# Kernel optimization log

Measured on AMD Instinct MI355X. Metric: run time of the kernel, lower is better.

The kernel has to match this reference:

```python
import jax, jax.numpy as jnp
import numpy as np

N_NODES = 100000
N_EDGES = 3200000
EMBED = 64
DIMS = [(64, 32), (32, 16)]  # (in_dim, out_dim) per Aggregator layer
EPS = 1e-12


def setup_inputs() -> dict:
    key = jax.random.key(0)
    ks = jax.random.split(key, 16)
    inp = {
        "aux_info_all": jax.random.normal(ks[0], (N_NODES, 3), jnp.float32),
        "entity_embed": jax.random.normal(ks[1], (N_NODES, EMBED), jnp.float32) * 0.1,
        "aux_W": jax.random.normal(ks[2], (EMBED, 3), jnp.float32) * 0.3,
        "aux_b": jnp.zeros((EMBED,), jnp.float32),
        "edge_vals": jax.random.uniform(ks[3], (N_EDGES,), jnp.float32),
        "edge_rows": jax.random.randint(ks[4], (N_EDGES,), 0, N_NODES, jnp.int32),
        "edge_cols": jax.random.randint(ks[5], (N_EDGES,), 0, N_NODES, jnp.int32),
    }
    for li, (din, dout) in enumerate(DIMS):
        s = (2.0 / (din + dout)) ** 0.5  # xavier-ish scale
        inp[f"W1_{li}"] = jax.random.normal(ks[6 + 4 * li], (dout, din), jnp.float32) * s
        inp[f"b1_{li}"] = jnp.zeros((dout,), jnp.float32)
        inp[f"W2_{li}"] = jax.random.normal(ks[7 + 4 * li], (dout, din), jnp.float32) * s
        inp[f"b2_{li}"] = jnp.zeros((dout,), jnp.float32)
    return inp


def _l2norm(x):
    return x / jnp.maximum(jnp.linalg.norm(x, axis=1, keepdims=True), EPS)


def reference(aux_info_all, entity_embed, aux_W, aux_b,
              W1_0, b1_0, W2_0, b2_0, W1_1, b1_1, W2_1, b2_1,
              edge_vals, edge_rows, edge_cols):
    # holographic fusion: entity_embed * (1 + tanh(Linear(aux)))
    aux_vec = jnp.tanh(aux_info_all @ aux_W.T + aux_b)
    ego = entity_embed * (1.0 + aux_vec)  # [N, 64]
    all_embed = [ego]
    layers = [(W1_0, b1_0, W2_0, b2_0), (W1_1, b1_1, W2_1, b2_1)]
    for W1, b1, W2, b2 in layers:
        # sparse A_in @ ego: gather messages over edges, segment-sum by destination row
        msgs = edge_vals[:, None] * ego[edge_cols]  # [E, d]
        side = jax.ops.segment_sum(msgs, edge_rows, num_segments=N_NODES)  # [N, d]
        sum_e = jax.nn.leaky_relu((ego + side) @ W1.T + b1)  # bi-interaction branch 1
        bi_e = jax.nn.leaky_relu((ego * side) @ W2.T + b2)   # bi-interaction branch 2
        ego = sum_e + bi_e  # (dropout p=0 in eval)
        all_embed.append(_l2norm(ego))
    return jnp.concatenate(all_embed, axis=1)  # [N, 64+32+16]
```

## Files before the change

### kernel.cpp

```cpp
#include <hip/hip_runtime.h>
#include <math.h>

#define NN 100000
#define NE 3200000
#define OUTD 112
#define BROWS 512
#define NBUCK 196
#define FILL_CH 8192
#define FILL_B ((NE + FILL_CH - 1) / FILL_CH)
#define BLD1_T 1024
#define SORT_T 512

__device__ inline unsigned short f32_to_bf16(float f) {
    unsigned u = __float_as_uint(f);
    u += 0x7FFFu + ((u >> 16) & 1u);
    return (unsigned short)(u >> 16);
}
__device__ inline float bf16_bits_to_f32(unsigned b) {
    return __uint_as_float(b << 16);
}

__global__ void fuse_ego_kernel(const float* __restrict__ aux_info,
                                const float* __restrict__ entity,
                                const float* __restrict__ aux_W,
                                const float* __restrict__ aux_b,
                                unsigned short* __restrict__ ego0h,
                                float* __restrict__ out) {
    int idx = blockIdx.x * blockDim.x + threadIdx.x;
    if (idx >= NN * 64) return;
    int n = idx >> 6;
    int j = idx & 63;
    float a0 = aux_info[n * 3 + 0];
    float a1 = aux_info[n * 3 + 1];
    float a2 = aux_info[n * 3 + 2];
    float w0 = aux_W[j * 3 + 0];
    float w1 = aux_W[j * 3 + 1];
    float w2 = aux_W[j * 3 + 2];
    float t = tanhf(fmaf(a0, w0, fmaf(a1, w1, fmaf(a2, w2, aux_b[j]))));
    float e = entity[idx] * (1.0f + t);
    ego0h[idx] = f32_to_bf16(e);
    out[(size_t)n * OUTD + j] = e;
}

__global__ void bhist_kernel(const int* __restrict__ rows, int* __restrict__ gcount) {
    __shared__ int h[NBUCK];
    for (int i = threadIdx.x; i < NBUCK; i += BLD1_T) h[i] = 0;
    __syncthreads();
    int base = blockIdx.x * FILL_CH;
    int nE = NE - base; if (nE > FILL_CH) nE = FILL_CH;
    for (int i = threadIdx.x; i < nE; i += BLD1_T)
        atomicAdd(&h[rows[base + i] >> 9], 1);
    __syncthreads();
    for (int i = threadIdx.x; i < NBUCK; i += BLD1_T)
        if (h[i]) atomicAdd(&gcount[i], h[i]);
}

__global__ void bscan_kernel(const int* __restrict__ gcount,
                             int* __restrict__ bucket_base,
                             int* __restrict__ gcursor) {
    __shared__ int sh[256];
    int t = threadIdx.x;
    int v = (t < NBUCK) ? gcount[t] : 0;
    sh[t] = v;
    __syncthreads();
    for (int off = 1; off < 256; off <<= 1) {
        int u = (t >= off) ? sh[t - off] : 0;
        __syncthreads();
        sh[t] += u;
        __syncthreads();
    }
    if (t < NBUCK) {
        int excl = sh[t] - v;
        bucket_base[t] = excl;
        gcursor[t] = excl;
    }
    if (t == 255) bucket_base[NBUCK] = sh[255];
}

__global__ void bucket_fill_kernel(const int* __restrict__ rows,
                                   const int* __restrict__ cols,
                                   const float* __restrict__ vals,
                                   int* __restrict__ gcursor,
                                   int2* __restrict__ edges_b) {
    __shared__ int rowsL[FILL_CH];
    __shared__ int hcnt[NBUCK];
    __shared__ int curs[NBUCK];
    int base = blockIdx.x * FILL_CH;
    int nE = NE - base; if (nE > FILL_CH) nE = FILL_CH;
    for (int i = threadIdx.x; i < NBUCK; i += BLD1_T) hcnt[i] = 0;
    __syncthreads();
    for (int i = threadIdx.x; i < nE; i += BLD1_T) {
        int r = rows[base + i];
        rowsL[i] = r;
        atomicAdd(&hcnt[r >> 9], 1);
    }
    __syncthreads();
    for (int b = threadIdx.x; b < NBUCK; b += BLD1_T) {
        int c = hcnt[b];
        curs[b] = c ? atomicAdd(&gcursor[b], c) : 0;
    }
    __syncthreads();
    for (int i = threadIdx.x; i < nE; i += BLD1_T) {
        int r = rowsL[i];
        int b = r >> 9;
        int p = atomicAdd(&curs[b], 1);
        edges_b[p] = make_int2(cols[base + i] | ((r & (BROWS - 1)) << 17),
                               __float_as_int(vals[base + i]));
    }
}

__global__ void csr_sort_kernel(const int2* __restrict__ edges_b,
                                const int* __restrict__ bucket_base,
                                unsigned int* __restrict__ edges,
                                int* __restrict__ row_ptr) {
    __shared__ int cnt[BROWS];
    __shared__ int scn[BROWS];
    __shared__ int curs[BROWS];
    int b = blockIdx.x;
    int beg = bucket_base[b], end = bucket_base[b + 1];
    int t = threadIdx.x;
    cnt[t] = 0;
    __syncthreads();
    for (int i = beg + t; i < end; i += SORT_T)
        atomicAdd(&cnt[(edges_b[i].x >> 17) & (BROWS - 1)], 1);
    __syncthreads();
    scn[t] = cnt[t];
    __syncthreads();
    for (int off = 1; off < BROWS; off <<= 1) {
        int v = (t >= off) ? scn[t - off] : 0;
        __syncthreads();
        scn[t] += v;
        __syncthreads();
    }
    {
        int excl = scn[t] - cnt[t];
        int n = b * BROWS + t;
        if (n <= NN) row_ptr[n] = beg + excl;
        curs[t] = beg + excl;
    }
    __syncthreads();
    for (int i = beg + t; i < end; i += SORT_T) {
        int2 e = edges_b[i];
        int rl = (e.x >> 17) & (BROWS - 1);
        int p = atomicAdd(&curs[rl], 1);
        unsigned int vb = f32_to_bf16(__int_as_float(e.y)) & 0x7FFFu;
        edges[p] = (unsigned int)(e.x & 0x1FFFF) | (vb << 17);
    }
}

template <int D>
__global__ void gather_kernel(const ushort2* __restrict__ egoh,
                              const unsigned int* __restrict__ edges,
                              const int* __restrict__ row_ptr,
                              float* __restrict__ side) {
    constexpr int L = D / 2;
    int n = blockIdx.x * (256 / L) + threadIdx.x / L;
    int j = threadIdx.x % L;
    if (n >= NN) return;
    int beg = row_ptr[n];
    int end = row_ptr[n + 1];
    float a0 = 0.0f, a1 = 0.0f;
    int i = beg;
    for (; i + 16 <= end; i += 16) {
        unsigned int e[16];
        ushort2 gv[16];
#pragma unroll
        for (int k = 0; k < 16; ++k) e[k] = edges[i + k];
#pragma unroll
        for (int k = 0; k < 16; ++k) gv[k] = egoh[(size_t)(e[k] & 0x1FFFFu) * L + j];
#pragma unroll
        for (int k = 0; k < 16; ++k) {
            float v = bf16_bits_to_f32(e[k] >> 17);
            a0 = fmaf(v, bf16_bits_to_f32(gv[k].x), a0);
            a1 = fmaf(v, bf16_bits_to_f32(gv[k].y), a1);
        }
    }
    for (; i + 8 <= end; i += 8) {
        unsigned int e[8];
        ushort2 gv[8];
#pragma unroll
        for (int k = 0; k < 8; ++k) e[k] = edges[i + k];
#pragma unroll
        for (int k = 0; k < 8; ++k) gv[k] = egoh[(size_t)(e[k] & 0x1FFFFu) * L + j];
#pragma unroll
        for (int k = 0; k < 8; ++k) {
            float v = bf16_bits_to_f32(e[k] >> 17);
            a0 = fmaf(v, bf16_bits_to_f32(gv[k].x), a0);
            a1 = fmaf(v, bf16_bits_to_f32(gv[k].y), a1);
        }
    }
    for (; i < end; ++i) {
        unsigned int e = edges[i];
        ushort2 g = egoh[(size_t)(e & 0x1FFFFu) * L + j];
        float v = bf16_bits_to_f32(e >> 17);
        a0 = fmaf(v, bf16_bits_to_f32(g.x), a0);
        a1 = fmaf(v, bf16_bits_to_f32(g.y), a1);
    }
    side[(size_t)n * D + 2 * j]     = a0;
    side[(size_t)n * D + 2 * j + 1] = a1;
}

template <int DIN, int DOUT, int NB>
__global__ __launch_bounds__(256, 4) void layer_kernel(
    const float* __restrict__ ego, int ego_stride,
    const float* __restrict__ side,
    const float* __restrict__ W1, const float* __restrict__ b1,
    const float* __restrict__ W2, const float* __restrict__ b2,
    float* __restrict__ ego_next,
    unsigned short* __restrict__ ego_next_h,
    float* __restrict__ out, int out_off)
{
    constexpr int RW  = DIN + 4;
    constexpr int CH  = DIN / 4;
    constexpr int NPT = NB * DOUT / 256;
    static_assert(NB * DOUT % 256 == 0, "");
    static_assert(NPT == 4, "register budget tuned for NPT=4");

    __shared__ float sArr[NB][RW];
    __shared__ float pArr[NB][RW];
    __shared__ float4 W1q[CH * DOUT];
    __shared__ float4 W2q[CH * DOUT];

    const int node0 = blockIdx.x * NB;

    for (int t = threadIdx.x; t < CH * DOUT; t += 256) {
        int j  = t / CH;
        int kg = t - j * CH;
        W1q[kg * DOUT + j] = *(const float4*)&W1[j * DIN + kg * 4];
        W2q[kg * DOUT + j] = *(const float4*)&W2[j * DIN + kg * 4];
    }

    for (int i = threadIdx.x; i < NB * CH; i += 256) {
        int m = i / CH;
        int c = i - m * CH;
        int n = node0 + m;
        if (n < NN) {
            float4 e  = *(const float4*)&ego[(size_t)n * ego_stride + c * 4];
            float4 sd = *(const float4*)&side[(size_t)n * DIN + c * 4];
            *(float4*)&sArr[m][c * 4] =
                make_float4(e.x + sd.x, e.y + sd.y, e.z + sd.z, e.w + sd.w);
            *(float4*)&pArr[m][c * 4] =
                make_float4(e.x * sd.x, e.y * sd.y, e.z * sd.z, e.w * sd.w);
        }
    }
    __syncthreads();

    const int j     = threadIdx.x % DOUT;
    const int slot  = threadIdx.x / DOUT;
    const int mbase = slot * NPT;

    float acc1[NPT], acc2[NPT];
    {
        float bb1 = b1[j], bb2 = b2[j];
#pragma unroll
        for (int m8 = 0; m8 < NPT; ++m8) { acc1[m8] = bb1; acc2[m8] = bb2; }
    }

#pragma unroll 2
    for (int kg = 0; kg < CH; ++kg) {
        float4 w1 = W1q[kg * DOUT + j];
        float4 w2 = W2q[kg * DOUT + j];
#pragma unroll
        for (int m8 = 0; m8 < NPT; ++m8) {
            float4 sv = *(const float4*)&sArr[mbase + m8][kg * 4];
            float4 pv = *(const float4*)&pArr[mbase + m8][kg * 4];
            acc1[m8] = fmaf(sv.x, w1.x, acc1[m8]);
            acc1[m8] = fmaf(sv.y, w1.y, acc1[m8]);
            acc1[m8] = fmaf(sv.z, w1.z, acc1[m8]);
            acc1[m8] = fmaf(sv.w, w1.w, acc1[m8]);
            acc2[m8] = fmaf(pv.x, w2.x, acc2[m8]);
            acc2[m8] = fmaf(pv.y, w2.y, acc2[m8]);
            acc2[m8] = fmaf(pv.z, w2.z, acc2[m8]);
            acc2[m8] = fmaf(pv.w, w2.w, acc2[m8]);
        }
    }

#pragma unroll
    for (int m8 = 0; m8 < NPT; ++m8) {
        int n = node0 + mbase + m8;
        float s  = acc1[m8]; s  = (s  > 0.0f) ? s  : 0.01f * s;
        float bb = acc2[m8]; bb = (bb > 0.0f) ? bb : 0.01f * bb;
        float v = s + bb;
        float sq = v * v;
#pragma unroll
        for (int off = DOUT / 2; off > 0; off >>= 1)
            sq += __shfl_xor(sq, off, DOUT);
        float norm = sqrtf(sq);
        norm = (norm > 1e-12f) ? norm : 1e-12f;
        if (n < NN) {
            if (ego_next)   ego_next[(size_t)n * DOUT + j] = v;
            if (ego_next_h) ego_next_h[(size_t)n * DOUT + j] = f32_to_bf16(v);
            out[(size_t)n * OUTD + out_off + j] = v / norm;
        }
    }
}

extern "C" void kernel_launch(void* const* d_in, const int* in_sizes, int n_in,
                              void* d_out, int out_size, void* d_ws, size_t ws_size,
                              hipStream_t stream) {
    const float* aux_info  = (const float*)d_in[0];
    const float* entity    = (const float*)d_in[1];
    const float* aux_W     = (const float*)d_in[2];
    const float* aux_b     = (const float*)d_in[3];
    const float* edge_vals = (const float*)d_in[4];
    const int*   edge_rows = (const int*)d_in[5];
    const int*   edge_cols = (const int*)d_in[6];
    const float* W1_0 = (const float*)d_in[7];
    const float* b1_0 = (const float*)d_in[8];
    const float* W2_0 = (const float*)d_in[9];
    const float* b2_0 = (const float*)d_in[10];
    const float* W1_1 = (const float*)d_in[11];
    const float* b1_1 = (const float*)d_in[12];
    const float* W2_1 = (const float*)d_in[13];
    const float* b2_1 = (const float*)d_in[14];
    float* out = (float*)d_out;

    float* region0 = (float*)d_ws;
    int2*  edges_b = (int2*)region0;
    float* side0   = region0;
    unsigned short* ego0h = (unsigned short*)(region0 + (size_t)NE * 2);
    unsigned short* ego1h = ego0h;
    unsigned int* edges = (unsigned int*)((float*)ego0h + (size_t)NN * 32);
    float* ego1  = (float*)(edges + NE);
    float* side1 = ego1 + (size_t)NN * 32;
    int* row_ptr     = (int*)(side1 + (size_t)NN * 32);
    int* bucket_base = row_ptr + NN + 1;
    int* gcount      = bucket_base + NBUCK + 1;

    hipMemsetAsync(gcount, 0, (size_t)NBUCK * sizeof(int), stream);
    bhist_kernel<<<FILL_B, BLD1_T, 0, stream>>>(edge_rows, gcount);
    bscan_kernel<<<1, 256, 0, stream>>>(gcount, bucket_base, gcount);
    bucket_fill_kernel<<<FILL_B, BLD1_T, 0, stream>>>(
        edge_rows, edge_cols, edge_vals, gcount, edges_b);
    csr_sort_kernel<<<NBUCK, SORT_T, 0, stream>>>(edges_b, bucket_base, edges, row_ptr);

    {
        int total = NN * 64;
        fuse_ego_kernel<<<(total + 255) / 256, 256, 0, stream>>>(
            aux_info, entity, aux_W, aux_b, ego0h, out);
    }
    gather_kernel<64><<<(NN + 7) / 8, 256, 0, stream>>>(
        (const ushort2*)ego0h, edges, row_ptr, side0);
    layer_kernel<64, 32, 32><<<(NN + 31) / 32, 256, 0, stream>>>(
        out, OUTD, side0, W1_0, b1_0, W2_0, b2_0, ego1, ego1h, out, 64);
    gather_kernel<32><<<(NN + 15) / 16, 256, 0, stream>>>(
        (const ushort2*)ego1h, edges, row_ptr, side1);
    layer_kernel<32, 16, 64><<<(NN + 63) / 64, 256, 0, stream>>>(
        ego1, 32, side1, W1_1, b1_1, W2_1, b2_1, nullptr, nullptr, out, 96);
}
```

Measured before the change: 398.2 us.

## Restructure CSR gather to 16-byte loads with edge-parallel lanes and shuffle reduction

Each destination row is now handled by 32 lanes. Every lane loads 16-byte chunks, 8 bf16 features each, from the source node, and different lane groups process different edges of the row at the same time. Partial sums are combined with xor shuffles and written back as float4 stores. The aim is more memory-level parallelism and fewer, wider load instructions per edge in the dominant sparse gather. The cost is a cross-lane reduction and more accumulator registers per lane.

```diff
diff --git a/kernel.cpp b/kernel.cpp
--- a/kernel.cpp
+++ b/kernel.cpp
@@ -149,55 +149,82 @@
 }
 
 template <int D>
-__global__ void gather_kernel(const ushort2* __restrict__ egoh,
-                              const unsigned int* __restrict__ edges,
-                              const int* __restrict__ row_ptr,
-                              float* __restrict__ side) {
-    constexpr int L = D / 2;
-    int n = blockIdx.x * (256 / L) + threadIdx.x / L;
-    int j = threadIdx.x % L;
+__global__ __launch_bounds__(256) void gather_kernel(
+    const uint4* __restrict__ egoh4,
+    const unsigned int* __restrict__ edges,
+    const int* __restrict__ row_ptr,
+    float* __restrict__ side) {
+    constexpr int FO = D / 8;
+    constexpr int ES = 32 / FO;
+    constexpr int U  = 16 / ES;
+    const int gt = blockIdx.x * 256 + threadIdx.x;
+    const int n  = gt >> 5;
+    const int li = gt & 31;
+    const int es = li / FO;
+    const int fo = li % FO;
     if (n >= NN) return;
     int beg = row_ptr[n];
     int end = row_ptr[n + 1];
-    float a0 = 0.0f, a1 = 0.0f;
+    float a[8] = {0.f, 0.f, 0.f, 0.f, 0.f, 0.f, 0.f, 0.f};
     int i = beg;
-    for (; i + 16 <= end; i += 16) {
-        unsigned int e[16];
-        ushort2 gv[16];
-#pragma unroll
-        for (int k = 0; k < 16; ++k) e[k] = edges[i + k];
-#pragma unroll
-        for (int k = 0; k < 16; ++k) gv[k] = egoh[(size_t)(e[k] & 0x1FFFFu) * L + j];
-#pragma unroll
-        for (int k = 0; k < 16; ++k) {
-            float v = bf16_bits_to_f32(e[k] >> 17);
-            a0 = fmaf(v, bf16_bits_to_f32(gv[k].x), a0);
-            a1 = fmaf(v, bf16_bits_to_f32(gv[k].y), a1);
+    for (; i + U * ES <= end; i += U * ES) {
+        unsigned ew[U];
+        uint4 g[U];
+#pragma unroll
+        for (int u = 0; u < U; ++u) ew[u] = edges[i + u * ES + es];
+#pragma unroll
+        for (int u = 0; u < U; ++u)
+            g[u] = egoh4[(size_t)(ew[u] & 0x1FFFFu) * FO + fo];
+#pragma unroll
+        for (int u = 0; u < U; ++u) {
+            float v = __uint_as_float((ew[u] >> 1) & 0xFFFF0000u);
+            a[0] = fmaf(v, __uint_as_float(g[u].x << 16), a[0]);
+            a[1] = fmaf(v, __uint_as_float(g[u].x & 0xFFFF0000u), a[1]);
+            a[2] = fmaf(v, __uint_as_float(g[u].y << 16), a[2]);
+            a[3] = fmaf(v, __uint_as_float(g[u].y & 0xFFFF0000u), a[3]);
+            a[4] = fmaf(v, __uint_as_float(g[u].z << 16), a[4]);
+            a[5] = fmaf(v, __uint_as_float(g[u].z & 0xFFFF0000u), a[5]);
+            a[6] = fmaf(v, __uint_as_float(g[u].w << 16), a[6]);
+            a[7] = fmaf(v, __uint_as_float(g[u].w & 0xFFFF0000u), a[7]);
         }
     }
-    for (; i + 8 <= end; i += 8) {
-        unsigned int e[8];
-        ushort2 gv[8];
-#pragma unroll
-        for (int k = 0; k < 8; ++k) e[k] = edges[i + k];
-#pragma unroll
-        for (int k = 0; k < 8; ++k) gv[k] = egoh[(size_t)(e[k] & 0x1FFFFu) * L + j];
-#pragma unroll
-        for (int k = 0; k < 8; ++k) {
-            float v = bf16_bits_to_f32(e[k] >> 17);
-            a0 = fmaf(v, bf16_bits_to_f32(gv[k].x), a0);
-            a1 = fmaf(v, bf16_bits_to_f32(gv[k].y), a1);
-        }
-    }
-    for (; i < end; ++i) {
-        unsigned int e = edges[i];
-        ushort2 g = egoh[(size_t)(e & 0x1FFFFu) * L + j];
-        float v = bf16_bits_to_f32(e >> 17);
-        a0 = fmaf(v, bf16_bits_to_f32(g.x), a0);
-        a1 = fmaf(v, bf16_bits_to_f32(g.y), a1);
-    }
-    side[(size_t)n * D + 2 * j]     = a0;
-    side[(size_t)n * D + 2 * j + 1] = a1;
+    for (; i + ES <= end; i += ES) {
+        unsigned ew = edges[i + es];
+        uint4 g = egoh4[(size_t)(ew & 0x1FFFFu) * FO + fo];
+        float v = __uint_as_float((ew >> 1) & 0xFFFF0000u);
+        a[0] = fmaf(v, __uint_as_float(g.x << 16), a[0]);
+        a[1] = fmaf(v, __uint_as_float(g.x & 0xFFFF0000u), a[1]);
+        a[2] = fmaf(v, __uint_as_float(g.y << 16), a[2]);
+        a[3] = fmaf(v, __uint_as_float(g.y & 0xFFFF0000u), a[3]);
+        a[4] = fmaf(v, __uint_as_float(g.z << 16), a[4]);
+        a[5] = fmaf(v, __uint_as_float(g.z & 0xFFFF0000u), a[5]);
+        a[6] = fmaf(v, __uint_as_float(g.w << 16), a[6]);
+        a[7] = fmaf(v, __uint_as_float(g.w & 0xFFFF0000u), a[7]);
+    }
+    if (i + es < end) {
+        unsigned ew = edges[i + es];
+        uint4 g = egoh4[(size_t)(ew & 0x1FFFFu) * FO + fo];
+        float v = __uint_as_float((ew >> 1) & 0xFFFF0000u);
+        a[0] = fmaf(v, __uint_as_float(g.x << 16), a[0]);
+        a[1] = fmaf(v, __uint_as_float(g.x & 0xFFFF0000u), a[1]);
+        a[2] = fmaf(v, __uint_as_float(g.y << 16), a[2]);
+        a[3] = fmaf(v, __uint_as_float(g.y & 0xFFFF0000u), a[3]);
+        a[4] = fmaf(v, __uint_as_float(g.z << 16), a[4]);
+        a[5] = fmaf(v, __uint_as_float(g.z & 0xFFFF0000u), a[5]);
+        a[6] = fmaf(v, __uint_as_float(g.w << 16), a[6]);
+        a[7] = fmaf(v, __uint_as_float(g.w & 0xFFFF0000u), a[7]);
+    }
+#pragma unroll
+    for (int st = FO; st < 32; st <<= 1) {
+#pragma unroll
+        for (int q = 0; q < 8; ++q) a[q] += __shfl_xor(a[q], st);
+    }
+    if (es == 0)
+        *(float4*)&side[(size_t)n * D + fo * 8] =
+            make_float4(a[0], a[1], a[2], a[3]);
+    else if (es == 1)
+        *(float4*)&side[(size_t)n * D + fo * 8 + 4] =
+            make_float4(a[4], a[5], a[6], a[7]);
 }
 
 template <int DIN, int DOUT, int NB>
@@ -339,12 +366,12 @@
         fuse_ego_kernel<<<(total + 255) / 256, 256, 0, stream>>>(
             aux_info, entity, aux_W, aux_b, ego0h, out);
     }
-    gather_kernel<64><<<(NN + 7) / 8, 256, 0, stream>>>(
-        (const ushort2*)ego0h, edges, row_ptr, side0);
+    gather_kernel<64><<<NN / 8, 256, 0, stream>>>(
+        (const uint4*)ego0h, edges, row_ptr, side0);
     layer_kernel<64, 32, 32><<<(NN + 31) / 32, 256, 0, stream>>>(
         out, OUTD, side0, W1_0, b1_0, W2_0, b2_0, ego1, ego1h, out, 64);
-    gather_kernel<32><<<(NN + 15) / 16, 256, 0, stream>>>(
-        (const ushort2*)ego1h, edges, row_ptr, side1);
+    gather_kernel<32><<<NN / 8, 256, 0, stream>>>(
+        (const uint4*)ego1h, edges, row_ptr, side1);
     layer_kernel<32, 16, 64><<<(NN + 63) / 64, 256, 0, stream>>>(
         ego1, 32, side1, W1_1, b1_1, W2_1, b2_1, nullptr, nullptr, out, 96);
 }
```

New measurement: 385.1 us. 3.3% less time.
